# Performance work log

Measured on AMD Instinct MI355X. Metric: run time of the kernel, lower is better.

Reference implementation:

```python
import jax, jax.numpy as jnp
import numpy as np

H = 1024  # lstm_hidden_dim

def setup_inputs() -> dict:
    key = jax.random.key(0)
    ks = jax.random.split(key, 8)
    T, E, V = 2048, 512, 32000
    return {
        "sentence": jax.random.randint(ks[0], (1, T), 0, V, dtype=jnp.int32),
        "emb": jax.random.normal(ks[1], (V, E), dtype=jnp.float32) * 0.1,
        "Wi": jax.random.normal(ks[2], (E, 4 * H), dtype=jnp.float32) * (1.0 / np.sqrt(H)),
        "Wh": jax.random.normal(ks[3], (H, 4 * H), dtype=jnp.float32) * (1.0 / np.sqrt(H)),
        "bi": jax.random.normal(ks[4], (4 * H,), dtype=jnp.float32) * 0.01,
        "bh": jax.random.normal(ks[5], (4 * H,), dtype=jnp.float32) * 0.01,
        "fc_w": jax.random.normal(ks[6], (V, H), dtype=jnp.float32) * (1.0 / np.sqrt(H)),
        "fc_b": jnp.zeros((V,), dtype=jnp.float32),
    }

def _lstm(x, Wi, Wh, bi, bh):
    # x: (T, E). Batch is 1 in the original (input viewed as (1, -1, E)).
    # Precompute input contribution for all timesteps (hoists the big GEMM out of the loop).
    xg = x @ Wi + bi + bh  # (T, 4H)

    def step(carry, g):
        h, c = carry  # (H,), (H,)
        gates = g + h @ Wh  # (4H,)
        i_g, f_g, c_g, o_g = jnp.split(gates, 4)
        i_g = jax.nn.sigmoid(i_g)
        f_g = jax.nn.sigmoid(f_g)
        c_g = jnp.tanh(c_g)
        o_g = jax.nn.sigmoid(o_g)
        c = f_g * c + i_g * c_g
        h = o_g * jnp.tanh(c)
        return (h, c), h

    init = (jnp.zeros((Wh.shape[0],), x.dtype), jnp.zeros((Wh.shape[0],), x.dtype))
    _, hs = jax.lax.scan(step, init, xg)  # hs: (T, H)
    return hs

def reference(sentence, emb, Wi, Wh, bi, bh, fc_w, fc_b):
    x = emb[sentence.reshape(-1)]  # (T, E)
    hs = _lstm(x, Wi, Wh, bi, bh)  # (T, H)
    logits = jax.nn.relu(hs @ fc_w.T + fc_b)  # (T, V)
    return jax.nn.log_softmax(logits, axis=1)  # is_test=False path
```

## Files before the change

### kernel.cpp

```cpp
#include <hip/hip_runtime.h>
#include <hip/hip_bf16.h>
#include <cmath>

#define T_LEN 2048
#define E_DIM 512
#define H_DIM 1024
#define G_DIM 4096
#define V_DIM 32000
#define LSTM_NB 256
#define NREP 8
#define RING 4

typedef unsigned short ushortx8 __attribute__((ext_vector_type(8)));
typedef unsigned short ushortx4 __attribute__((ext_vector_type(4)));
typedef short shortx8 __attribute__((ext_vector_type(8)));
typedef float floatx4 __attribute__((ext_vector_type(4)));
typedef unsigned uintx4 __attribute__((ext_vector_type(4)));

__device__ __forceinline__ float bf2f(unsigned short u) {
    return __uint_as_float(((unsigned)u) << 16);
}
__device__ __forceinline__ unsigned short f2bf(float f) {
    __hip_bfloat16 b = __float2bfloat16(f);
    return *reinterpret_cast<unsigned short*>(&b);
}
__device__ __forceinline__ float fast_sigmoid(float x) {
    return 1.f / (1.f + __expf(-x));
}
__device__ __forceinline__ float fast_tanh(float x) {
    return 1.f - 2.f / (__expf(2.f * x) + 1.f);
}

__global__ __launch_bounds__(256) void prep_kernel(const float* __restrict__ Wh,
                                                   unsigned short* __restrict__ whTp)
{
    const int c0  = blockIdx.x * 16;
    const int tid = threadIdx.x;
    const int cc  = tid & 15;
    const int kk  = tid >> 4;
    const int col = c0 + cc;
    unsigned short* dst = whTp + (size_t)col * H_DIM;
    #pragma unroll 4
    for (int r = 0; r < 64; ++r) {
        const int i = r * 16 + kk;
        float v = Wh[(size_t)i * G_DIM + col];
        const int pos = ((i & 255) >> 2) * 16 + (i >> 8) * 4 + (i & 3);
        dst[pos] = f2bf(v);
    }
}

__global__ __launch_bounds__(256) void embconv_kernel(const float* __restrict__ src,
                                                      unsigned short* __restrict__ dst)
{
    const size_t i = ((size_t)blockIdx.x * 256 + threadIdx.x) * 8;
    float4 a = *reinterpret_cast<const float4*>(src + i);
    float4 b = *reinterpret_cast<const float4*>(src + i + 4);
    ushortx8 o;
    o[0] = f2bf(a.x); o[1] = f2bf(a.y); o[2] = f2bf(a.z); o[3] = f2bf(a.w);
    o[4] = f2bf(b.x); o[5] = f2bf(b.y); o[6] = f2bf(b.z); o[7] = f2bf(b.w);
    *reinterpret_cast<ushortx8*>(dst + i) = o;
}

__global__ __launch_bounds__(256) void wiconv_kernel(const float* __restrict__ Wi,
                                                     unsigned short* __restrict__ wiT)
{
    __shared__ float tile[32][33];
    const int nb = blockIdx.x * 32;
    const int kb = blockIdx.y * 32;
    const int tx = threadIdx.x & 31;
    const int ty = threadIdx.x >> 5;
    #pragma unroll
    for (int i = 0; i < 32; i += 8)
        tile[ty + i][tx] = Wi[(size_t)(kb + ty + i) * G_DIM + nb + tx];
    __syncthreads();
    #pragma unroll
    for (int i = 0; i < 32; i += 8)
        wiT[(size_t)(nb + ty + i) * E_DIM + kb + tx] = f2bf(tile[tx][ty + i]);
}

__global__ __launch_bounds__(256) void fcwconv_kernel(const float* __restrict__ src,
                                                      unsigned short* __restrict__ dst)
{
    const size_t i = ((size_t)blockIdx.x * 256 + threadIdx.x) * 8;
    float4 a = *reinterpret_cast<const float4*>(src + i);
    float4 b = *reinterpret_cast<const float4*>(src + i + 4);
    ushortx8 o;
    o[0] = f2bf(a.x); o[1] = f2bf(a.y); o[2] = f2bf(a.z); o[3] = f2bf(a.w);
    o[4] = f2bf(b.x); o[5] = f2bf(b.y); o[6] = f2bf(b.z); o[7] = f2bf(b.w);
    *reinterpret_cast<ushortx8*>(dst + i) = o;
}

__global__ __launch_bounds__(256) void xg_mfma_kernel(const int* __restrict__ sent,
                                                      const unsigned short* __restrict__ embb,
                                                      const unsigned short* __restrict__ wiT,
                                                      const float* __restrict__ bi,
                                                      const float* __restrict__ bh,
                                                      unsigned short* __restrict__ xg2)
{
    const int tid  = threadIdx.x;
    const int w    = tid >> 6;
    const int lane = tid & 63;
    const int n0 = blockIdx.x * 64;
    const int m0 = blockIdx.y * 128;
    const int lrow = lane & 15;
    const int lk   = (lane >> 4) * 8;

    const int r0 = sent[m0 + w * 32 + lrow];
    const int r1 = sent[m0 + w * 32 + 16 + lrow];

    floatx4 acc[2][4] = {};
    const unsigned short* a0p = embb + (size_t)r0 * E_DIM + lk;
    const unsigned short* a1p = embb + (size_t)r1 * E_DIM + lk;
    const unsigned short* b0p = wiT + (size_t)(n0 + lrow) * E_DIM + lk;

    for (int k0 = 0; k0 < E_DIM; k0 += 32) {
        shortx8 a0 = *reinterpret_cast<const shortx8*>(a0p + k0);
        shortx8 a1 = *reinterpret_cast<const shortx8*>(a1p + k0);
        shortx8 b0 = *reinterpret_cast<const shortx8*>(b0p + k0);
        shortx8 b1 = *reinterpret_cast<const shortx8*>(b0p + 16 * E_DIM + k0);
        shortx8 b2 = *reinterpret_cast<const shortx8*>(b0p + 32 * E_DIM + k0);
        shortx8 b3 = *reinterpret_cast<const shortx8*>(b0p + 48 * E_DIM + k0);
        acc[0][0] = __builtin_amdgcn_mfma_f32_16x16x32_bf16(a0, b0, acc[0][0], 0, 0, 0);
        acc[0][1] = __builtin_amdgcn_mfma_f32_16x16x32_bf16(a0, b1, acc[0][1], 0, 0, 0);
        acc[0][2] = __builtin_amdgcn_mfma_f32_16x16x32_bf16(a0, b2, acc[0][2], 0, 0, 0);
        acc[0][3] = __builtin_amdgcn_mfma_f32_16x16x32_bf16(a0, b3, acc[0][3], 0, 0, 0);
        acc[1][0] = __builtin_amdgcn_mfma_f32_16x16x32_bf16(a1, b0, acc[1][0], 0, 0, 0);
        acc[1][1] = __builtin_amdgcn_mfma_f32_16x16x32_bf16(a1, b1, acc[1][1], 0, 0, 0);
        acc[1][2] = __builtin_amdgcn_mfma_f32_16x16x32_bf16(a1, b2, acc[1][2], 0, 0, 0);
        acc[1][3] = __builtin_amdgcn_mfma_f32_16x16x32_bf16(a1, b3, acc[1][3], 0, 0, 0);
    }

    #pragma unroll
    for (int j = 0; j < 4; ++j) {
        const int c = n0 + j * 16 + lrow;
        const int hidx = c & 1023;
        const int gate = c >> 10;
        const float bias = bi[c] + bh[c];
        #pragma unroll
        for (int i = 0; i < 2; ++i) {
            #pragma unroll
            for (int reg = 0; reg < 4; ++reg) {
                const int r = m0 + w * 32 + i * 16 + (lane >> 4) * 4 + reg;
                xg2[(size_t)r * G_DIM + hidx * 4 + gate] = f2bf(acc[i][j][reg] + bias);
            }
        }
    }
}

__global__ __launch_bounds__(256) void lstm_kernel(const unsigned short* __restrict__ xg2,
                                                   const unsigned short* __restrict__ whTp,
                                                   unsigned* __restrict__ ring,
                                                   unsigned short* __restrict__ hb,
                                                   int T)
{
    const int b    = blockIdx.x;
    const int tid  = threadIdx.x;
    const int w    = tid >> 6;
    const int lane = tid & 63;
    const int s    = b * 4;
    const int rep  = b & (NREP - 1);

    __shared__ float h_lds[H_DIM];

    float c_val = 0.0f;

    for (int t = 0; t < T; ++t) {
        float xr[4] = {0.f, 0.f, 0.f, 0.f};
        if (lane == 0) {
            ushortx4 xv = *reinterpret_cast<const ushortx4*>(
                xg2 + (size_t)t * G_DIM + (size_t)(s + w) * 4);
            #pragma unroll
            for (int q = 0; q < 4; ++q) xr[q] = bf2f(xv[q]);
        }

        if (t) {
            const unsigned* pp = ring + ((t - 1) & (RING - 1)) * (NREP * H_DIM)
                                      + rep * H_DIM + tid * 4;
            const unsigned tg = (unsigned)t;
            uintx4 v;
            int guard = 0;
            bool ok;
            do {
                asm volatile("global_load_dwordx4 %0, %1, off sc0 sc1\n\t"
                             "s_waitcnt vmcnt(0)"
                             : "=&v"(v) : "v"(pp) : "memory");
                ok = ((v[0] >> 16) == tg) & ((v[1] >> 16) == tg)
                   & ((v[2] >> 16) == tg) & ((v[3] >> 16) == tg);
            } while (!ok && ++guard < 8192);
            floatx4 hv;
            hv[0] = __uint_as_float(v[0] << 16);
            hv[1] = __uint_as_float(v[1] << 16);
            hv[2] = __uint_as_float(v[2] << 16);
            hv[3] = __uint_as_float(v[3] << 16);
            *reinterpret_cast<floatx4*>(&h_lds[tid * 4]) = hv;
        } else {
            floatx4 z = {0.f, 0.f, 0.f, 0.f};
            *reinterpret_cast<floatx4*>(&h_lds[tid * 4]) = z;
        }
        __syncthreads();

        float hreg[16];
        #pragma unroll
        for (int c = 0; c < 4; ++c) {
            floatx4 hv = *reinterpret_cast<const floatx4*>(&h_lds[c * 256 + lane * 4]);
            hreg[c * 4 + 0] = hv[0]; hreg[c * 4 + 1] = hv[1];
            hreg[c * 4 + 2] = hv[2]; hreg[c * 4 + 3] = hv[3];
        }

        float sums[4];
        #pragma unroll
        for (int q = 0; q < 4; ++q) {
            const ushortx8* wp = reinterpret_cast<const ushortx8*>(
                whTp + ((size_t)((q << 10) + s + w)) * H_DIM + lane * 16);
            ushortx8 w0 = wp[0];
            ushortx8 w1 = wp[1];
            float sm = 0.f;
            #pragma unroll
            for (int e = 0; e < 8; ++e) sm += bf2f(w0[e]) * hreg[e];
            #pragma unroll
            for (int e = 0; e < 8; ++e) sm += bf2f(w1[e]) * hreg[8 + e];
            #pragma unroll
            for (int off = 32; off; off >>= 1) sm += __shfl_xor(sm, off, 64);
            sums[q] = sm;
        }

        if (lane == 0) {
            float ig = fast_sigmoid(sums[0] + xr[0]);
            float fg = fast_sigmoid(sums[1] + xr[1]);
            float gg = fast_tanh(sums[2] + xr[2]);
            float og = fast_sigmoid(sums[3] + xr[3]);
            c_val = fg * c_val + ig * gg;
            float h = og * fast_tanh(c_val);
            const unsigned short hbf = f2bf(h);
            const unsigned pk = ((unsigned)(t + 1) << 16) | (unsigned)hbf;
            unsigned* base = ring + (t & (RING - 1)) * (NREP * H_DIM) + s + w;
            #pragma unroll
            for (int r = 0; r < NREP; ++r) {
                unsigned* sp = base + r * H_DIM;
                asm volatile("global_store_dword %0, %1, off sc0 sc1"
                             :: "v"(sp), "v"(pk) : "memory");
            }
            hb[(size_t)t * H_DIM + s + w] = hbf;
        }
    }
}

__global__ __launch_bounds__(256) void fc_kernel(const unsigned short* __restrict__ hb,
                                                 const unsigned short* __restrict__ fcwb,
                                                 const float* __restrict__ fcb,
                                                 float* __restrict__ out)
{
    const int tid  = threadIdx.x;
    const int w    = tid >> 6;
    const int lane = tid & 63;
    const int n0 = blockIdx.x * 128;
    const int m0 = blockIdx.y * 256;
    const int lrow = lane & 15;
    const int lk   = (lane >> 4) * 8;

    floatx4 acc[4][8] = {};
    const unsigned short* ap = hb + (size_t)(m0 + w * 64 + lrow) * H_DIM + lk;
    const unsigned short* b0p = fcwb + (size_t)(n0 + lrow) * H_DIM + lk;

    for (int k0 = 0; k0 < H_DIM; k0 += 32) {
        shortx8 a0 = *reinterpret_cast<const shortx8*>(ap + k0);
        shortx8 a1 = *reinterpret_cast<const shortx8*>(ap + 16 * H_DIM + k0);
        shortx8 a2 = *reinterpret_cast<const shortx8*>(ap + 32 * H_DIM + k0);
        shortx8 a3 = *reinterpret_cast<const shortx8*>(ap + 48 * H_DIM + k0);
        #pragma unroll
        for (int j = 0; j < 8; ++j) {
            shortx8 bj = *reinterpret_cast<const shortx8*>(b0p + j * 16 * H_DIM + k0);
            acc[0][j] = __builtin_amdgcn_mfma_f32_16x16x32_bf16(a0, bj, acc[0][j], 0, 0, 0);
            acc[1][j] = __builtin_amdgcn_mfma_f32_16x16x32_bf16(a1, bj, acc[1][j], 0, 0, 0);
            acc[2][j] = __builtin_amdgcn_mfma_f32_16x16x32_bf16(a2, bj, acc[2][j], 0, 0, 0);
            acc[3][j] = __builtin_amdgcn_mfma_f32_16x16x32_bf16(a3, bj, acc[3][j], 0, 0, 0);
        }
    }

    #pragma unroll
    for (int j = 0; j < 8; ++j) {
        const int c = n0 + j * 16 + lrow;
        const float bias = fcb[c];
        #pragma unroll
        for (int i = 0; i < 4; ++i) {
            #pragma unroll
            for (int reg = 0; reg < 4; ++reg) {
                const int r = m0 + w * 64 + i * 16 + (lane >> 4) * 4 + reg;
                out[(size_t)r * V_DIM + c] = fmaxf(acc[i][j][reg] + bias, 0.f);
            }
        }
    }
}

__global__ __launch_bounds__(256) void lsm_kernel(float* __restrict__ out)
{
    const int row = blockIdx.x;
    float* p = out + (size_t)row * V_DIM;
    const int tid = threadIdx.x;
    __shared__ float ms[256], ss[256];

    float m = -1e30f, sacc = 0.f;
    for (int i4 = tid; i4 < V_DIM / 4; i4 += 256) {
        float4 v = *reinterpret_cast<const float4*>(p + i4 * 4);
        float vm = fmaxf(fmaxf(v.x, v.y), fmaxf(v.z, v.w));
        if (vm > m) { sacc *= __expf(m - vm); m = vm; }
        sacc += __expf(v.x - m) + __expf(v.y - m) + __expf(v.z - m) + __expf(v.w - m);
    }
    ms[tid] = m; ss[tid] = sacc; __syncthreads();
    for (int sft = 128; sft; sft >>= 1) {
        if (tid < sft) {
            float m2 = ms[tid + sft], s2 = ss[tid + sft];
            float mm = fmaxf(ms[tid], m2);
            ss[tid] = ss[tid] * __expf(ms[tid] - mm) + s2 * __expf(m2 - mm);
            ms[tid] = mm;
        }
        __syncthreads();
    }
    const float L = ms[0] + logf(ss[0]);

    for (int i4 = tid; i4 < V_DIM / 4; i4 += 256) {
        float4 v = *reinterpret_cast<const float4*>(p + i4 * 4);
        v.x -= L; v.y -= L; v.z -= L; v.w -= L;
        *reinterpret_cast<float4*>(p + i4 * 4) = v;
    }
}

extern "C" void kernel_launch(void* const* d_in, const int* in_sizes, int n_in,
                              void* d_out, int out_size, void* d_ws, size_t ws_size,
                              hipStream_t stream)
{
    const int*   sent = (const int*)  d_in[0];
    const float* emb  = (const float*)d_in[1];
    const float* Wi   = (const float*)d_in[2];
    const float* Wh   = (const float*)d_in[3];
    const float* bi   = (const float*)d_in[4];
    const float* bh   = (const float*)d_in[5];
    const float* fcw  = (const float*)d_in[6];
    const float* fcb  = (const float*)d_in[7];
    float* out = (float*)d_out;

    uint8_t* ws = (uint8_t*)d_ws;
    size_t off = 0;
    unsigned*       ring = (unsigned*)(ws + off);       off += (size_t)RING * NREP * H_DIM * 4;
    unsigned short* xg2  = (unsigned short*)(ws + off); off += (size_t)T_LEN * G_DIM * 2;
    unsigned short* whTp = (unsigned short*)(ws + off); off += (size_t)G_DIM * H_DIM * 2;
    unsigned short* hb   = (unsigned short*)(ws + off); off += (size_t)T_LEN * H_DIM * 2;
    uint8_t* R = ws + off;
    unsigned short* fcwb = (unsigned short*)R;
    unsigned short* embb = (unsigned short*)R;
    unsigned short* wiT  = (unsigned short*)(R + (size_t)V_DIM * E_DIM * 2);

    hipMemsetAsync(ring, 0, (size_t)RING * NREP * H_DIM * 4, stream);
    embconv_kernel<<<(int)(((size_t)V_DIM * E_DIM / 8) / 256), 256, 0, stream>>>(emb, embb);
    wiconv_kernel<<<dim3(G_DIM / 32, E_DIM / 32), 256, 0, stream>>>(Wi, wiT);
    prep_kernel<<<G_DIM / 16, 256, 0, stream>>>(Wh, whTp);
    xg_mfma_kernel<<<dim3(G_DIM / 64, T_LEN / 128), 256, 0, stream>>>(sent, embb, wiT, bi, bh, xg2);
    fcwconv_kernel<<<(int)(((size_t)V_DIM * H_DIM / 8) / 256), 256, 0, stream>>>(fcw, fcwb);
    lstm_kernel<<<LSTM_NB, 256, 0, stream>>>(xg2, whTp, ring, hb, T_LEN);
    fc_kernel<<<dim3(V_DIM / 128, T_LEN / 256), 256, 0, stream>>>(hb, fcwb, fcb, out);
    lsm_kernel<<<T_LEN, 256, 0, stream>>>(out);
}
```

Measured before the change: 5.239 ms.

## Merge weight-prep kernels and overlap fc_w conversion with the LSTM kernel

Folds the embedding, Wi and Wh bf16 conversion kernels into one launch that dispatches on block index. The fc_w fp32-to-bf16 conversion moves into extra blocks appended to the LSTM launch, using a grid-stride loop. The aim is to cut launch overhead and hide the bandwidth-bound conversion behind the latency-bound recurrent kernel. The risk is that the extra blocks compete with the persistent LSTM blocks for memory bandwidth and CU slots during the early timesteps.

```diff
diff --git a/kernel.cpp b/kernel.cpp
--- a/kernel.cpp
+++ b/kernel.cpp
@@ -8,6 +8,7 @@
 #define G_DIM 4096
 #define V_DIM 32000
 #define LSTM_NB 256
+#define FCONV_NB 512
 #define NREP 8
 #define RING 4
 
@@ -31,63 +32,56 @@
     return 1.f - 2.f / (__expf(2.f * x) + 1.f);
 }
 
-__global__ __launch_bounds__(256) void prep_kernel(const float* __restrict__ Wh,
-                                                   unsigned short* __restrict__ whTp)
-{
-    const int c0  = blockIdx.x * 16;
+#define PRE_EMB_NB   8000
+#define PRE_WI_NB    2048
+#define PRE_WH_NB    256
+__global__ __launch_bounds__(256) void preconv_kernel(const float* __restrict__ emb,
+                                                      unsigned short* __restrict__ embb,
+                                                      const float* __restrict__ Wi,
+                                                      unsigned short* __restrict__ wiT,
+                                                      const float* __restrict__ Wh,
+                                                      unsigned short* __restrict__ whTp)
+{
+    __shared__ float tile[32][33];
+    const int bid = blockIdx.x;
     const int tid = threadIdx.x;
-    const int cc  = tid & 15;
-    const int kk  = tid >> 4;
-    const int col = c0 + cc;
-    unsigned short* dst = whTp + (size_t)col * H_DIM;
-    #pragma unroll 4
-    for (int r = 0; r < 64; ++r) {
-        const int i = r * 16 + kk;
-        float v = Wh[(size_t)i * G_DIM + col];
-        const int pos = ((i & 255) >> 2) * 16 + (i >> 8) * 4 + (i & 3);
-        dst[pos] = f2bf(v);
-    }
-}
-
-__global__ __launch_bounds__(256) void embconv_kernel(const float* __restrict__ src,
-                                                      unsigned short* __restrict__ dst)
-{
-    const size_t i = ((size_t)blockIdx.x * 256 + threadIdx.x) * 8;
-    float4 a = *reinterpret_cast<const float4*>(src + i);
-    float4 b = *reinterpret_cast<const float4*>(src + i + 4);
-    ushortx8 o;
-    o[0] = f2bf(a.x); o[1] = f2bf(a.y); o[2] = f2bf(a.z); o[3] = f2bf(a.w);
-    o[4] = f2bf(b.x); o[5] = f2bf(b.y); o[6] = f2bf(b.z); o[7] = f2bf(b.w);
-    *reinterpret_cast<ushortx8*>(dst + i) = o;
-}
-
-__global__ __launch_bounds__(256) void wiconv_kernel(const float* __restrict__ Wi,
-                                                     unsigned short* __restrict__ wiT)
-{
-    __shared__ float tile[32][33];
-    const int nb = blockIdx.x * 32;
-    const int kb = blockIdx.y * 32;
-    const int tx = threadIdx.x & 31;
-    const int ty = threadIdx.x >> 5;
-    #pragma unroll
-    for (int i = 0; i < 32; i += 8)
-        tile[ty + i][tx] = Wi[(size_t)(kb + ty + i) * G_DIM + nb + tx];
-    __syncthreads();
-    #pragma unroll
-    for (int i = 0; i < 32; i += 8)
-        wiT[(size_t)(nb + ty + i) * E_DIM + kb + tx] = f2bf(tile[tx][ty + i]);
-}
-
-__global__ __launch_bounds__(256) void fcwconv_kernel(const float* __restrict__ src,
-                                                      unsigned short* __restrict__ dst)
-{
-    const size_t i = ((size_t)blockIdx.x * 256 + threadIdx.x) * 8;
-    float4 a = *reinterpret_cast<const float4*>(src + i);
-    float4 b = *reinterpret_cast<const float4*>(src + i + 4);
-    ushortx8 o;
-    o[0] = f2bf(a.x); o[1] = f2bf(a.y); o[2] = f2bf(a.z); o[3] = f2bf(a.w);
-    o[4] = f2bf(b.x); o[5] = f2bf(b.y); o[6] = f2bf(b.z); o[7] = f2bf(b.w);
-    *reinterpret_cast<ushortx8*>(dst + i) = o;
+
+    if (bid < PRE_EMB_NB) {
+        const size_t i = ((size_t)bid * 256 + tid) * 8;
+        float4 a = *reinterpret_cast<const float4*>(emb + i);
+        float4 b = *reinterpret_cast<const float4*>(emb + i + 4);
+        ushortx8 o;
+        o[0] = f2bf(a.x); o[1] = f2bf(a.y); o[2] = f2bf(a.z); o[3] = f2bf(a.w);
+        o[4] = f2bf(b.x); o[5] = f2bf(b.y); o[6] = f2bf(b.z); o[7] = f2bf(b.w);
+        *reinterpret_cast<ushortx8*>(embb + i) = o;
+    } else if (bid < PRE_EMB_NB + PRE_WI_NB) {
+        const int b2 = bid - PRE_EMB_NB;
+        const int nb = (b2 & 127) * 32;
+        const int kb = (b2 >> 7) * 32;
+        const int tx = tid & 31;
+        const int ty = tid >> 5;
+        #pragma unroll
+        for (int i = 0; i < 32; i += 8)
+            tile[ty + i][tx] = Wi[(size_t)(kb + ty + i) * G_DIM + nb + tx];
+        __syncthreads();
+        #pragma unroll
+        for (int i = 0; i < 32; i += 8)
+            wiT[(size_t)(nb + ty + i) * E_DIM + kb + tx] = f2bf(tile[tx][ty + i]);
+    } else {
+        const int b3 = bid - PRE_EMB_NB - PRE_WI_NB;
+        const int c0 = b3 * 16;
+        const int cc = tid & 15;
+        const int kk = tid >> 4;
+        const int col = c0 + cc;
+        unsigned short* dst = whTp + (size_t)col * H_DIM;
+        #pragma unroll 4
+        for (int r = 0; r < 64; ++r) {
+            const int i = r * 16 + kk;
+            float v = Wh[(size_t)i * G_DIM + col];
+            const int pos = ((i & 255) >> 2) * 16 + (i >> 8) * 4 + (i & 3);
+            dst[pos] = f2bf(v);
+        }
+    }
 }
 
 __global__ __launch_bounds__(256) void xg_mfma_kernel(const int* __restrict__ sent,
@@ -151,10 +145,28 @@
                                                    const unsigned short* __restrict__ whTp,
                                                    unsigned* __restrict__ ring,
                                                    unsigned short* __restrict__ hb,
+                                                   const float* __restrict__ fcw,
+                                                   unsigned short* __restrict__ fcwb,
                                                    int T)
 {
     const int b    = blockIdx.x;
     const int tid  = threadIdx.x;
+
+    if (b >= LSTM_NB) {
+        const size_t total  = (size_t)V_DIM * H_DIM;
+        const size_t stride = (size_t)FCONV_NB * 256 * 8;
+        size_t i = ((size_t)(b - LSTM_NB) * 256 + tid) * 8;
+        for (; i < total; i += stride) {
+            float4 a = *reinterpret_cast<const float4*>(fcw + i);
+            float4 v = *reinterpret_cast<const float4*>(fcw + i + 4);
+            ushortx8 o;
+            o[0] = f2bf(a.x); o[1] = f2bf(a.y); o[2] = f2bf(a.z); o[3] = f2bf(a.w);
+            o[4] = f2bf(v.x); o[5] = f2bf(v.y); o[6] = f2bf(v.z); o[7] = f2bf(v.w);
+            *reinterpret_cast<ushortx8*>(fcwb + i) = o;
+        }
+        return;
+    }
+
     const int w    = tid >> 6;
     const int lane = tid & 63;
     const int s    = b * 4;
@@ -351,12 +363,10 @@
     unsigned short* wiT  = (unsigned short*)(R + (size_t)V_DIM * E_DIM * 2);
 
     hipMemsetAsync(ring, 0, (size_t)RING * NREP * H_DIM * 4, stream);
-    embconv_kernel<<<(int)(((size_t)V_DIM * E_DIM / 8) / 256), 256, 0, stream>>>(emb, embb);
-    wiconv_kernel<<<dim3(G_DIM / 32, E_DIM / 32), 256, 0, stream>>>(Wi, wiT);
-    prep_kernel<<<G_DIM / 16, 256, 0, stream>>>(Wh, whTp);
+    preconv_kernel<<<PRE_EMB_NB + PRE_WI_NB + PRE_WH_NB, 256, 0, stream>>>(
+        emb, embb, Wi, wiT, Wh, whTp);
     xg_mfma_kernel<<<dim3(G_DIM / 64, T_LEN / 128), 256, 0, stream>>>(sent, embb, wiT, bi, bh, xg2);
-    fcwconv_kernel<<<(int)(((size_t)V_DIM * H_DIM / 8) / 256), 256, 0, stream>>>(fcw, fcwb);
-    lstm_kernel<<<LSTM_NB, 256, 0, stream>>>(xg2, whTp, ring, hb, T_LEN);
+    lstm_kernel<<<LSTM_NB + FCONV_NB, 256, 0, stream>>>(xg2, whTp, ring, hb, fcw, fcwb, T_LEN);
     fc_kernel<<<dim3(V_DIM / 128, T_LEN / 256), 256, 0, stream>>>(hb, fcwb, fcb, out);
     lsm_kernel<<<T_LEN, 256, 0, stream>>>(out);
 }
```

Measured after the change: 5.835 ms. 11.4% more time.
